# Performance work log

Measured on AMD Instinct MI355X. Metric: run time of the kernel, lower is better.

## Reference

```python
import jax, jax.numpy as jnp
import numpy as np
import math

B, C, N, T = 16, 32, 500, 10
NH, DK = 8, 8
D = NH * DK  # 64
TT = 6       # tem_size after conv_temp1 (10->6)
EPS = 1e-5


def setup_inputs() -> dict:
    key = jax.random.key(0)
    ks = jax.random.split(key, 32)
    s = 0.05
    rn = lambda k, shp: jax.random.normal(k, shp, dtype=jnp.float32) * s
    return {
        "x": jax.random.normal(ks[0], (B, C, N, T), dtype=jnp.float32),
        "A": jax.random.uniform(ks[1], (N, N), dtype=jnp.float32) / N,
        "conv1_W": rn(ks[2], (32, 32)), "conv1_b": jnp.zeros((32,), jnp.float32),
        "te1_W": rn(ks[3], (64, 32)), "te1_b": jnp.zeros((64,), jnp.float32),
        "convq_W": rn(ks[4], (64, 64, 1, 3)), "convq_b": jnp.zeros((64,), jnp.float32),
        "convk_W": rn(ks[5], (64, 64, 1, 3)), "convk_b": jnp.zeros((64,), jnp.float32),
        "linv_W": rn(ks[6], (64, 64)), "linv_b": jnp.zeros((64,), jnp.float32),
        "lino_W": rn(ks[7], (64, 64)), "lino_b": jnp.zeros((64,), jnp.float32),
        "te2_W": rn(ks[8], (32, 64)), "te2_b": jnp.zeros((32,), jnp.float32),
        "mlp_W": rn(ks[9], (64, 160)), "mlp_b": jnp.zeros((64,), jnp.float32),
        "ct1_W": rn(ks[10], (6, 10)), "ct1_b": jnp.zeros((6,), jnp.float32),
        "tat_c1_W": rn(ks[11], (32,)), "tat_c2_W": rn(ks[12], (500,)),
        "tat_w": rn(ks[13], (500, 32)), "tat_b": jnp.zeros((6, 6), jnp.float32),
        "tat_v": rn(ks[14], (6, 6)),
        "bn1_g": jnp.ones((6,), jnp.float32), "bn1_b": jnp.zeros((6,), jnp.float32),
        "bn2_g": jnp.ones((32,), jnp.float32), "bn2_b": jnp.zeros((32,), jnp.float32),
    }


def _forward(x, A, conv1_W, conv1_b, te1_W, te1_b, convq_W, convq_b, convk_W, convk_b,
             linv_W, linv_b, lino_W, lino_b, te2_W, te2_b, mlp_W, mlp_b, ct1_W, ct1_b,
             tat_c1_W, tat_c2_W, tat_w, tat_b, tat_v, bn1_g, bn1_b, bn2_g, bn2_b):
    b, c, n, t = x.shape
    c1x1 = lambda z, W, bb: jnp.einsum('bchw,oc->bohw', z, W) + bb[None, :, None, None]
    residual = c1x1(x, conv1_W, conv1_b)                      # (B,32,N,T)
    h = c1x1(x, te1_W, te1_b)                                 # (B,64,N,T)
    # --- temporal-context multi-head self-attention (att bias is 0 in source due to bug) ---
    dn = ('NCHW', 'OIHW', 'NCHW')
    q = jax.lax.conv_general_dilated(h, convq_W, (1, 1), ((0, 0), (1, 1)), dimension_numbers=dn) + convq_b[None, :, None, None]
    k = jax.lax.conv_general_dilated(h, convk_W, (1, 1), ((0, 0), (1, 1)), dimension_numbers=dn) + convk_b[None, :, None, None]
    sh = lambda z: z.reshape(b, NH, DK, n, t).transpose(0, 3, 1, 4, 2)  # (B,N,h,T,dk)
    q, k = sh(q), sh(k)
    hp = h.transpose(0, 2, 3, 1)                              # (B,N,T,64)
    v = (hp @ linv_W.T + linv_b).reshape(b, n, t, NH, DK).transpose(0, 1, 3, 2, 4)
    p = jax.nn.softmax(jnp.einsum('bnhtd,bnhsd->bnhts', q, k) / math.sqrt(DK), axis=-1)
    o = jnp.einsum('bnhts,bnhsd->bnhtd', p, v).transpose(0, 1, 3, 2, 4).reshape(b, n, t, D)
    h = (o @ lino_W.T + lino_b).transpose(0, 3, 1, 2)         # (B,64,N,T)
    h = c1x1(h, te2_W, te2_b)                                 # (B,32,N,T)
    # --- multi_gcn_d: static adjacency diffusion + per-timestep attention adjacency ---
    co = h.shape[1]
    xt = h.transpose(0, 3, 2, 1)                              # (B,T,N,C)
    att = jax.nn.softmax(jnp.einsum('btnc,btmc->btnm', xt, xt) / math.sqrt(co), axis=-1)
    outs = [h]
    z = jnp.einsum('btvc,wv->btwc', xt, A); outs.append(z.transpose(0, 3, 2, 1))
    z = jnp.einsum('btvc,wv->btwc', z, A);  outs.append(z.transpose(0, 3, 2, 1))
    z = jnp.einsum('btvc,btwv->btwc', xt, att); outs.append(z.transpose(0, 3, 2, 1))
    z = jnp.einsum('btvc,btwv->btwc', z, att);  outs.append(z.transpose(0, 3, 2, 1))
    hc = c1x1(jnp.concatenate(outs, axis=1), mlp_W, mlp_b)    # (B,64,N,T)
    g = jnp.tanh(hc[:, :co]) * jax.nn.sigmoid(hc[:, co:])     # (B,32,N,10)
    # --- conv_temp1: 1x1 conv over the time axis, 10 -> 6 ---
    g = jnp.einsum('bcnt,st->bcns', g, ct1_W) + ct1_b[None, None, None, :]  # (B,32,N,6)
    # --- TATT_1 temporal attention coefficients ---
    f1 = jnp.einsum('bcnt,c->btn', g, tat_c1_W)               # (B,6,N)
    f2 = jnp.einsum('bcnt,n->bct', g, tat_c2_W)               # (B,32,6)
    logits = jax.nn.sigmoid(jnp.einsum('btn,nc,bcs->bts', f1, tat_w, f2) + tat_b)
    logits = jnp.einsum('pt,bts->bps', tat_v, logits)         # (B,6,6)
    lp = logits.transpose(0, 2, 1)
    mu = lp.mean((0, 2), keepdims=True); var = lp.var((0, 2), keepdims=True)
    lp = (lp - mu) / jnp.sqrt(var + EPS) * bn1_g[None, :, None] + bn1_b[None, :, None]
    coefs = jax.nn.softmax(lp.transpose(0, 2, 1), axis=-1)    # (B,6,6)
    Tc = coefs.transpose(0, 2, 1)
    xo = jnp.einsum('bcnl,blq->bcnq', g, Tc)                  # (B,32,N,6)
    xo = jnp.where(xo > 0, xo, 0.01 * xo) + residual[..., -xo.shape[-1]:]
    mu = xo.mean((0, 2, 3), keepdims=True); var = xo.var((0, 2, 3), keepdims=True)
    return (xo - mu) / jnp.sqrt(var + EPS) * bn2_g[None, :, None, None] + bn2_b[None, :, None, None]


def reference(x, A, conv1_W, conv1_b, te1_W, te1_b, convq_W, convq_b, convk_W, convk_b,
              linv_W, linv_b, lino_W, lino_b, te2_W, te2_b, mlp_W, mlp_b, ct1_W, ct1_b,
              tat_c1_W, tat_c2_W, tat_w, tat_b, tat_v, bn1_g, bn1_b, bn2_g, bn2_b):
    return _forward(x, A, conv1_W, conv1_b, te1_W, te1_b, convq_W, convq_b, convk_W, convk_b,
                    linv_W, linv_b, lino_W, lino_b, te2_W, te2_b, mlp_W, mlp_b, ct1_W, ct1_b,
                    tat_c1_W, tat_c2_W, tat_w, tat_b, tat_v, bn1_g, bn1_b, bn2_g, bn2_b)
```

## Files before the change

kernel.cpp:

```cpp
#include <hip/hip_runtime.h>

typedef unsigned short u16;
typedef unsigned int u32;

__device__ __forceinline__ float b2f(u16 v) { return __uint_as_float((u32)v << 16); }
__device__ __forceinline__ float lopart(u32 u) { return __uint_as_float(u << 16); }
__device__ __forceinline__ float hipart(u32 u) { return __uint_as_float(u & 0xffff0000u); }
__device__ __forceinline__ u16 f2b(float f) {
  u32 u = __float_as_uint(f);
  u32 r = u + 0x7fffu + ((u >> 16) & 1u);
  return (u16)(r >> 16);
}
__device__ __forceinline__ u32 pk2(float a, float b) {
  return (u32)f2b(a) | ((u32)f2b(b) << 16);
}
__device__ __forceinline__ u32 cvtpk(float lo, float hi) {
  u32 r;
  asm("v_cvt_pk_bf16_f32 %0, %1, %2" : "=v"(r) : "v"(lo), "v"(hi));
  return r;
}
__device__ __forceinline__ float rd(const void* p, int i, bool BF) {
  return BF ? b2f(((const u16*)p)[i]) : ((const float*)p)[i];
}

struct Ptrs { const void* p[29]; };

typedef __attribute__((ext_vector_type(8))) short short8;
typedef __attribute__((ext_vector_type(4))) float floatx4;

__global__ __launch_bounds__(256) void k_prep(Ptrs ps, float* __restrict__ Wf,
                                              u16* __restrict__ Abf, float* __restrict__ WT,
                                              u16* __restrict__ WBu, float* __restrict__ stats) {
  bool BF = ((*(const u32*)ps.p[25]) & 0xffffu) != 0;
  int blk = blockIdx.x, tid = threadIdx.x;
  const void* p2  = ps.p[2];
  const void* p4  = ps.p[4];
  const void* p5  = ps.p[5];
  const void* p6  = ps.p[6];
  const void* p7  = ps.p[7];
  const void* p8  = ps.p[8];
  const void* p9  = ps.p[9];
  const void* p10 = ps.p[10];
  const void* p11 = ps.p[11];
  const void* p12 = ps.p[12];
  const void* p13 = ps.p[13];
  const void* p14 = ps.p[14];
  const void* p15 = ps.p[15];
  const void* p16 = ps.p[16];
  if (blk < 256) {
    int j = blk * 256 + tid;
    if (j >= 65322) return;
    const int SZ[27] = {1024,32,2048,64,12288,64,12288,64,4096,64,4096,64,2048,32,
                        10240,64,60,6,32,500,16000,36,36,6,6,32,32};
    int t = 0, off = 0;
#pragma unroll
    for (int k = 0; k < 27; ++k) {
      if (t == k && j >= off + SZ[k]) { off += SZ[k]; t = k + 1; }
    }
    Wf[j] = rd(ps.p[2 + t], j - off, BF);
  } else if (blk < 1280) {
    int i = (blk - 256) * 256 + tid;
    int r = i >> 9, v = i & 511;
    bool in = (r < 500) && (v < 500);
    u16 o = 0;
    if (in) o = BF ? ((const u16*)ps.p[1])[r * 500 + v] : f2b(((const float*)ps.p[1])[r * 500 + v]);
    Abf[i] = o;
  } else if (blk < 1366) {
    int i = (blk - 1280) * 256 + tid;
    if (i < 1024) {
      WT[i] = rd(p2, (i & 31) * 32 + (i >> 5), BF);
    } else if (i >= 9600 && i < 9664) {
      int o = i - 9600;
      float s = rd(p11, o, BF);
      for (int i2 = 0; i2 < 64; ++i2)
        s += rd(p10, o * 64 + i2, BF) * rd(p5, i2, BF);
      WT[i] = s;
    } else if (i >= 9664 && i < 11712) {
      int j2 = i - 9664;
      int jj = j2 >> 5, c = j2 & 31;
      float s = 0.f;
      for (int o2 = 0; o2 < 64; ++o2)
        s += rd(p14, c * 64 + o2, BF) * rd(p12, o2 * 64 + jj, BF);
      WT[i] = s;
    } else if (i >= 11712 && i < 11744) {
      int c = i - 11712;
      float s = rd(p15, c, BF);
      for (int o2 = 0; o2 < 64; ++o2)
        s += rd(p14, c * 64 + o2, BF) * rd(p13, o2, BF);
      WT[i] = s;
    } else if (i >= 11744 && i < 21984) {
      int j2 = i - 11744;
      int j = j2 & 7, lanev = (j2 >> 3) & 63, ct = (j2 >> 9) & 3, kt = j2 >> 11;
      int qv = lanev >> 4, lnv = lanev & 15;
      int o = ct * 16 + lnv, k = kt * 32 + qv * 8 + j;
      WBu[j2] = f2b(rd(p16, o * 160 + k, BF));
    }
  } else if (blk < 1390) {
    int idx = (blk - 1366) * 256 + tid;
    int i2 = idx & 3, lanev = (idx >> 2) & 63, mt = (idx >> 8) & 7, ks = idx >> 11;
    int q2 = lanev >> 4, ln = lanev & 15;
    int o = (mt & 3) * 16 + ln;
    const void* src = (mt >= 4) ? p8 : p6;
    int kb0 = q2 * 8 + 2 * i2;
    float v0 = 0.f, v1 = 0.f;
    for (int i3 = 0; i3 < 64; ++i3) {
      float w = rd(src, o * 192 + i3 * 3 + ks, BF);
      v0 += w * rd(p4, i3 * 32 + kb0, BF);
      v1 += w * rd(p4, i3 * 32 + kb0 + 1, BF);
    }
    ((u32*)WT)[22016 + idx] = pk2(v0, v1);
  } else if (blk < 1394) {
    int idx = (blk - 1390) * 256 + tid;
    int i2 = idx & 3, lanev = (idx >> 2) & 63, mt = idx >> 8;
    int o = mt * 16 + (lanev & 15);
    int kb0 = (lanev >> 4) * 8 + 2 * i2;
    float v0 = 0.f, v1 = 0.f;
    for (int i3 = 0; i3 < 64; ++i3) {
      float w = rd(p10, o * 64 + i3, BF);
      v0 += w * rd(p4, i3 * 32 + kb0, BF);
      v1 += w * rd(p4, i3 * 32 + kb0 + 1, BF);
    }
    ((u32*)WT)[28160 + idx] = pk2(v0, v1);
  } else if (blk < 1397) {
    int j = (blk - 1394) * 256 + tid;
    if (j < 768) {
      bool isK = j >= 384;
      int jj = isK ? j - 384 : j;
      int cls = jj >> 6, o = jj & 63;
      const void* srcW = isK ? p8 : p6;
      const void* srcB = isK ? p9 : p7;
      float S0 = 0.f, S1 = 0.f, S2 = 0.f;
      for (int i3 = 0; i3 < 64; ++i3) {
        float tb = rd(p5, i3, BF);
        S0 += rd(srcW, o * 192 + i3 * 3 + 0, BF) * tb;
        S1 += rd(srcW, o * 192 + i3 * 3 + 1, BF) * tb;
        S2 += rd(srcW, o * 192 + i3 * 3 + 2, BF) * tb;
      }
      float val = rd(srcB, o, BF) + S1 + (cls > 0 ? S0 : 0.f) + (cls < 2 ? S2 : 0.f);
      WT[29184 + j] = val;
    }
  } else {
    if (tid < 64) stats[tid] = 0.f;
  }
}

__global__ __launch_bounds__(256, 4) void k_a2m(const u16* __restrict__ Abf,
                                                u16* __restrict__ A2bf) {
  __shared__ u32 blsT[8192];
  int tid = threadIdx.x;
  int c0 = blockIdx.x * 32;
  for (int i = tid; i < 8192; i += 256) {
    int c = i & 31, h = i >> 5;
    int r0 = 2 * h;
    u32 lo = Abf[r0 * 512 + c0 + c];
    u32 hi = Abf[(r0 + 1) * 512 + c0 + c];
    blsT[c * 256 + (((h & 0xFC) ^ ((c & 15) << 2)) | (h & 3))] = lo | (hi << 16);
  }
  __syncthreads();
  int lane = tid & 63, wave = tid >> 6;
  int q = lane >> 4, ln = lane & 15;
  int rbase = blockIdx.y * 64 + wave * 16;
  const u32* Au = (const u32*)Abf;
  int arow = (rbase + ln) * 256;
  union F8 { u32 u[4]; short8 s; };
  floatx4 acc[2] = {{0.f,0.f,0.f,0.f},{0.f,0.f,0.f,0.f}};
  for (int c2 = 0; c2 < 16; ++c2) {
    int hb = c2 * 16 + q * 4;
    F8 af;
#pragma unroll
    for (int i2 = 0; i2 < 4; ++i2) af.u[i2] = Au[arow + hb + i2];
#pragma unroll
    for (int t2 = 0; t2 < 2; ++t2) {
      int c = t2 * 16 + ln;
      int baseT = c * 256 + (hb ^ ((c & 15) << 2));
      F8 bf;
#pragma unroll
      for (int i2 = 0; i2 < 4; ++i2) bf.u[i2] = blsT[baseT + i2];
      acc[t2] = __builtin_amdgcn_mfma_f32_16x16x32_bf16(af.s, bf.s, acc[t2], 0, 0, 0);
    }
  }
#pragma unroll
  for (int t2 = 0; t2 < 2; ++t2) {
#pragma unroll
    for (int i2 = 0; i2 < 4; ++i2) {
      int r = rbase + q * 4 + i2;
      A2bf[r * 512 + c0 + t2 * 16 + ln] = f2b(acc[t2][i2]);
    }
  }
}

__global__ __launch_bounds__(256, 5) void k_front3(
    const void* __restrict__ xraw, const void* __restrict__ g1, const float* __restrict__ WT,
    const float* __restrict__ c1B,
    float* __restrict__ h3x, float* __restrict__ res6)
{
  __shared__ __align__(16) float arena[4][1680];
  int tid = threadIdx.x;
  int wave = tid >> 6, lane = tid & 63;
  float* Aw = arena[wave];
  int pair = blockIdx.x * 4 + wave;
  int b = pair / 500, n = pair - b * 500;

  const float* c1T  = WT;
  const float* bvp  = WT + 9600;
  const float* otT  = WT + 9664;
  const float* botp = WT + 11712;
  const u32* WQKf = (const u32*)WT + 22016;
  const u32* WVf  = (const u32*)WT + 28160;
  const float* bq3 = WT + 29184;
  const float* bk3 = WT + 29568;

  {
    bool BF = ((*(const u32*)g1) & 0xffffu) != 0;
    int c0 = lane >> 1, hf = (lane & 1) * 5;
    int base = ((b * 32 + c0) * 500 + n) * 10 + hf;
    float* dst = Aw + c0 * 12 + hf;
    if (BF) {
      const u16* xp = (const u16*)xraw + base;
#pragma unroll
      for (int k2 = 0; k2 < 5; ++k2) dst[k2] = b2f(xp[k2]);
    } else {
      const float* xp = (const float*)xraw + base;
#pragma unroll
      for (int k2 = 0; k2 < 5; ++k2) dst[k2] = xp[k2];
    }
  }
  __builtin_amdgcn_wave_barrier();

  int cl = lane & 31, th = lane >> 5;
  int q2 = lane >> 4, ln15 = lane & 15;

  {
    float r0 = c1B[cl], r1 = r0, r2 = r0;
#pragma unroll 4
    for (int i = 0; i < 32; ++i) {
      float w = c1T[i * 32 + cl];
      const float* xr = Aw + i * 12 + 4 + th * 3;
      r0 += w * xr[0]; r1 += w * xr[1]; r2 += w * xr[2];
    }
    float* rp = res6 + ((b * 32 + cl) * 500 + n) * 6 + th * 3;
    rp[0] = r0; rp[1] = r1; rp[2] = r2;
  }

  {
    u32* xT3u = (u32*)Aw + 384;
    for (int e = lane; e < 480; e += 64) {
      int t = e / 48, col2 = e - t * 48;
      int kk0 = col2 * 2, kk1 = kk0 + 1;
      int tau0 = kk0 >> 5, c0 = kk0 & 31;
      int tau1 = kk1 >> 5, c1 = kk1 & 31;
      int tx0 = t - 1 + tau0, tx1 = t - 1 + tau1;
      float f0 = (tx0 >= 0 && tx0 < 10) ? Aw[c0 * 12 + tx0] : 0.f;
      float f1 = (tx1 >= 0 && tx1 < 10) ? Aw[c1 * 12 + tx1] : 0.f;
      xT3u[t * 52 + col2] = cvtpk(f0, f1);
    }
  }
  __builtin_amdgcn_wave_barrier();

  union F8 { u32 u[4]; short8 s; };
  floatx4 aq[4] = {{0.f,0.f,0.f,0.f},{0.f,0.f,0.f,0.f},{0.f,0.f,0.f,0.f},{0.f,0.f,0.f,0.f}};
  floatx4 ak[4] = {{0.f,0.f,0.f,0.f},{0.f,0.f,0.f,0.f},{0.f,0.f,0.f,0.f},{0.f,0.f,0.f,0.f}};
  floatx4 av[4] = {{0.f,0.f,0.f,0.f},{0.f,0.f,0.f,0.f},{0.f,0.f,0.f,0.f},{0.f,0.f,0.f,0.f}};
  {
    const u32* xT3u = (const u32*)Aw + 384;
#pragma unroll
    for (int ks = 0; ks < 3; ++ks) {
      F8 bfr;
      const u32* bp = xT3u + ln15 * 52 + ks * 16 + q2 * 4;
#pragma unroll
      for (int i2 = 0; i2 < 4; ++i2) bfr.u[i2] = bp[i2];
#pragma unroll
      for (int mt = 0; mt < 4; ++mt) {
        F8 afr;
        const u32* ap = WQKf + ((ks * 8 + mt) * 64 + lane) * 4;
#pragma unroll
        for (int i2 = 0; i2 < 4; ++i2) afr.u[i2] = ap[i2];
        aq[mt] = __builtin_amdgcn_mfma_f32_16x16x32_bf16(afr.s, bfr.s, aq[mt], 0, 0, 0);
      }
#pragma unroll
      for (int mt = 0; mt < 4; ++mt) {
        F8 afr;
        const u32* ap = WQKf + ((ks * 8 + 4 + mt) * 64 + lane) * 4;
#pragma unroll
        for (int i2 = 0; i2 < 4; ++i2) afr.u[i2] = ap[i2];
        ak[mt] = __builtin_amdgcn_mfma_f32_16x16x32_bf16(afr.s, bfr.s, ak[mt], 0, 0, 0);
      }
      if (ks == 1) {
#pragma unroll
        for (int mt = 0; mt < 4; ++mt) {
          F8 afr;
          const u32* ap = WVf + (mt * 64 + lane) * 4;
#pragma unroll
          for (int i2 = 0; i2 < 4; ++i2) afr.u[i2] = ap[i2];
          av[mt] = __builtin_amdgcn_mfma_f32_16x16x32_bf16(afr.s, bfr.s, av[mt], 0, 0, 0);
        }
      }
    }
  }
  __builtin_amdgcn_wave_barrier();
  if (ln15 < 10) {
    int t = ln15;
    int cls = (t == 0) ? 0 : ((t == 9) ? 2 : 1);
    const float* bq = bq3 + cls * 64;
    const float* bk = bk3 + cls * 64;
    u16* q16 = (u16*)Aw;
    u16* k16 = (u16*)((u32*)Aw + 320);
    u16* v16 = (u16*)((u32*)Aw + 960);
#pragma unroll
    for (int mt = 0; mt < 4; ++mt) {
#pragma unroll
      for (int i2 = 0; i2 < 4; ++i2) {
        int o = mt * 16 + q2 * 4 + i2;
        q16[o * 10 + t] = f2b(aq[mt][i2] + bq[o]);
        k16[o * 10 + t] = f2b(ak[mt][i2] + bk[o]);
        v16[o * 10 + t] = f2b(av[mt][i2] + bvp[o]);
      }
    }
  }
  __builtin_amdgcn_wave_barrier();

  {
    const u32* qb = (const u32*)Aw;
    const u32* kb = (const u32*)Aw + 320;
#pragma unroll
    for (int pass = 0; pass < 2; ++pass) {
      int row = pass * 64 + lane;
      if (row < 80) {
        int h8 = (row / 10) * 8, r = row - (row / 10) * 10;
        int rm = r >> 1, rs = r & 1;
        float sv[10];
#pragma unroll
        for (int s = 0; s < 10; ++s) sv[s] = 0.f;
#pragma unroll 2
        for (int d = 0; d < 8; ++d) {
          int jj = h8 + d;
          u32 qu = qb[jj * 5 + rm];
          float qv = rs ? hipart(qu) : lopart(qu);
          const u32* kp2 = kb + jj * 5;
          u32 ka0 = kp2[0], ka1 = kp2[1], ka2 = kp2[2], ka3 = kp2[3], ka4 = kp2[4];
          sv[0] += qv * lopart(ka0); sv[1] += qv * hipart(ka0);
          sv[2] += qv * lopart(ka1); sv[3] += qv * hipart(ka1);
          sv[4] += qv * lopart(ka2); sv[5] += qv * hipart(ka2);
          sv[6] += qv * lopart(ka3); sv[7] += qv * hipart(ka3);
          sv[8] += qv * lopart(ka4); sv[9] += qv * hipart(ka4);
        }
        const float sc_ = 0.35355339059327373f;
        float mx = sv[0];
#pragma unroll
        for (int s = 1; s < 10; ++s) mx = fmaxf(mx, sv[s]);
        float tot = 0.f, ev[10];
#pragma unroll
        for (int s = 0; s < 10; ++s) { ev[s] = __expf((sv[s] - mx) * sc_); tot += ev[s]; }
        float inv = 1.f / tot;
        u32* pp = (u32*)Aw + 1280 + row * 5;
#pragma unroll
        for (int m2 = 0; m2 < 5; ++m2)
          pp[m2] = cvtpk(ev[2 * m2] * inv, ev[2 * m2 + 1] * inv);
      }
    }
  }
  __builtin_amdgcn_wave_barrier();

  {
    float vrL[10];
    const u32* vp = (const u32*)Aw + 960 + lane * 5;
#pragma unroll
    for (int m2 = 0; m2 < 5; ++m2) {
      u32 w = vp[m2];
      vrL[2 * m2] = lopart(w); vrL[2 * m2 + 1] = hipart(w);
    }
    const u32* pb = (const u32*)Aw + 1280 + (lane >> 3) * 50;
    float orr[10];
#pragma unroll
    for (int t = 0; t < 10; ++t) {
      const u32* pr = pb + t * 5;
      float a = 0.f;
#pragma unroll
      for (int m2 = 0; m2 < 5; ++m2) {
        u32 w = pr[m2];
        a += lopart(w) * vrL[2 * m2] + hipart(w) * vrL[2 * m2 + 1];
      }
      orr[t] = a;
    }
    float* op = Aw + lane * 12;
    *(float4*)op       = make_float4(orr[0], orr[1], orr[2], orr[3]);
    *(float4*)(op + 4) = make_float4(orr[4], orr[5], orr[6], orr[7]);
    *(float2*)(op + 8) = make_float2(orr[8], orr[9]);
  }
  __builtin_amdgcn_wave_barrier();

  {
    float bt2 = botp[cl];
    float a5[5];
#pragma unroll
    for (int k2 = 0; k2 < 5; ++k2) a5[k2] = bt2;
    const float* tp0 = otT + cl;
    const float* base = Aw + th * 5;
#pragma unroll 2
    for (int j = 0; j < 64; ++j) {
      float w = tp0[j * 32];
      const float* lp = base + j * 12;
#pragma unroll
      for (int k2 = 0; k2 < 5; ++k2) a5[k2] += w * lp[k2];
    }
    int t0 = th * 5;
#pragma unroll
    for (int k2 = 0; k2 < 5; ++k2)
      h3x[((b * 10 + t0 + k2) * 500 + n) * 32 + cl] = a5[k2];
  }
}

__global__ __launch_bounds__(256, 4) void k_z12m(const float* __restrict__ h3x,
    const u16* __restrict__ Abf, const u16* __restrict__ A2bf,
    float* __restrict__ z1x, float* __restrict__ z2x) {
  __shared__ u32 xlsT[8192];
  int tid = threadIdx.x, bt = blockIdx.x;
  const float* src = h3x + bt * 16000;
  for (int i = tid; i < 8192; i += 256) {
    int n = i & 31, h = i >> 5;
    int r0 = 2 * h;
    float v0 = (r0 < 500) ? src[r0 * 32 + n] : 0.f;
    float v1 = (r0 + 1 < 500) ? src[(r0 + 1) * 32 + n] : 0.f;
    xlsT[n * 256 + (((h & 0xFC) ^ ((n & 15) << 2)) | (h & 3))] = cvtpk(v0, v1);
  }
  __syncthreads();
  int lane = tid & 63, wave = tid >> 6;
  int q = lane >> 4, ln = lane & 15;
  int rbase = blockIdx.y * 64 + wave * 16;
  const u32* Au = (const u32*)Abf;
  const u32* A2u = (const u32*)A2bf;
  int arow = (rbase + ln) * 256;
  union F8 { u32 u[4]; short8 s; };
  floatx4 acc1[2] = {{0.f,0.f,0.f,0.f},{0.f,0.f,0.f,0.f}};
  floatx4 acc2[2] = {{0.f,0.f,0.f,0.f},{0.f,0.f,0.f,0.f}};
  for (int c2 = 0; c2 < 16; ++c2) {
    int hb = c2 * 16 + q * 4;
    F8 a1f, a2f;
#pragma unroll
    for (int i2 = 0; i2 < 4; ++i2) {
      a1f.u[i2] = Au[arow + hb + i2];
      a2f.u[i2] = A2u[arow + hb + i2];
    }
#pragma unroll
    for (int t2 = 0; t2 < 2; ++t2) {
      int n = t2 * 16 + ln;
      int baseT = n * 256 + (hb ^ ((n & 15) << 2));
      F8 bf;
#pragma unroll
      for (int i2 = 0; i2 < 4; ++i2) bf.u[i2] = xlsT[baseT + i2];
      acc1[t2] = __builtin_amdgcn_mfma_f32_16x16x32_bf16(a1f.s, bf.s, acc1[t2], 0, 0, 0);
      acc2[t2] = __builtin_amdgcn_mfma_f32_16x16x32_bf16(a2f.s, bf.s, acc2[t2], 0, 0, 0);
    }
  }
  int outb = bt * 16000;
#pragma unroll
  for (int t2 = 0; t2 < 2; ++t2) {
#pragma unroll
    for (int i2 = 0; i2 < 4; ++i2) {
      int r = rbase + q * 4 + i2;
      if (r < 500) {
        z1x[outb + r * 32 + t2 * 16 + ln] = acc1[t2][i2];
        z2x[outb + r * 32 + t2 * 16 + ln] = acc2[t2][i2];
      }
    }
  }
}

__global__ __launch_bounds__(256, 2) void k_attn2(const float* __restrict__ keys,
                                                  const float* __restrict__ vals,
                                                  float* __restrict__ outp) {
  __shared__ u32 kls[10240];
  __shared__ u32 vls[8192];
  __shared__ u32 aux[1216];
  int tid = threadIdx.x, bt = blockIdx.x, yh = blockIdx.y;
  const float* kb = keys + bt * 16000;
  const float* vb = vals + bt * 16000;
  for (int i = tid; i < 8192; i += 256) {
    int r = i >> 4, cu = i & 15;
    float2 g = make_float2(0.f, 0.f);
    if (r < 500) g = *(const float2*)(kb + r * 32 + cu * 2);
    kls[r * 20 + cu] = cvtpk(g.x, g.y);
    int n = i & 31, h = i >> 5;
    int r0 = 2 * h;
    float v0 = (r0 < 500) ? vb[r0 * 32 + n] : 0.f;
    float v1 = (r0 + 1 < 500) ? vb[(r0 + 1) * 32 + n] : 0.f;
    vls[n * 256 + (((h & 0xFC) ^ ((n & 15) << 2)) | (h & 3))] = cvtpk(v0, v1);
  }
  __syncthreads();
  int lane = tid & 63, wave = tid >> 6;
  int q = lane >> 4, ln = lane & 15;
  int wrow = wave >> 1, ch = wave & 1;
  float* smx = (float*)(aux + 1088);
  float* sms = (float*)(aux + 1152);
  u32* myp = aux + wave * 272;
  float* zex = (float*)aux;
  u16* pw = (u16*)myp;
  union F8 { u32 u[4]; short8 s; };
  const float sc = 0.17677669529663687f;
  int outb = bt * 16000;
  for (int chunk = 0; chunk < 8; ++chunk) {
    int rbase = yh * 256 + chunk * 32 + wrow * 16;
    F8 af;
    {
      int r = rbase + ln;
      int wbase = r * 20 + q * 4;
#pragma unroll
      for (int i2 = 0; i2 < 4; ++i2)
        af.u[i2] = kls[wbase + i2];
    }
    floatx4 acc[16];
#pragma unroll
    for (int ctl = 0; ctl < 16; ++ctl) {
      int r2 = (ch * 16 + ctl) * 16 + ln;
      int wb2 = r2 * 20 + q * 4;
      F8 bf;
#pragma unroll
      for (int i2 = 0; i2 < 4; ++i2)
        bf.u[i2] = kls[wb2 + i2];
      acc[ctl] = __builtin_amdgcn_mfma_f32_16x16x32_bf16(af.s, bf.s,
                (floatx4){0.f, 0.f, 0.f, 0.f}, 0, 0, 0);
    }
    if (ch == 1 && ln >= 4) {
#pragma unroll
      for (int i2 = 0; i2 < 4; ++i2) acc[15][i2] = -1e30f;
    }
    float m[4];
#pragma unroll
    for (int i2 = 0; i2 < 4; ++i2) {
      float mm = -1e30f;
#pragma unroll
      for (int ctl = 0; ctl < 16; ++ctl) mm = fmaxf(mm, acc[ctl][i2]);
#pragma unroll
      for (int d = 1; d < 16; d <<= 1) mm = fmaxf(mm, __shfl_xor(mm, d));
      m[i2] = mm;
    }
    if (ln == 0) {
#pragma unroll
      for (int i2 = 0; i2 < 4; ++i2) smx[wave * 16 + q * 4 + i2] = m[i2];
    }
    __syncthreads();
    float sp[4];
#pragma unroll
    for (int i2 = 0; i2 < 4; ++i2) {
      float mm = fmaxf(m[i2], smx[(wave ^ 1) * 16 + q * 4 + i2]);
      float s = 0.f;
#pragma unroll
      for (int ctl = 0; ctl < 16; ++ctl) {
        float e = __expf((acc[ctl][i2] - mm) * sc);
        acc[ctl][i2] = e; s += e;
      }
#pragma unroll
      for (int d = 1; d < 16; d <<= 1) s += __shfl_xor(s, d);
      sp[i2] = s;
    }
    if (ln == 0) {
#pragma unroll
      for (int i2 = 0; i2 < 4; ++i2) sms[wave * 16 + q * 4 + i2] = sp[i2];
    }
    __syncthreads();
    float inv[4];
#pragma unroll
    for (int i2 = 0; i2 < 4; ++i2)
      inv[i2] = 1.f / (sp[i2] + sms[(wave ^ 1) * 16 + q * 4 + i2]);
    floatx4 zacc[2] = {{0.f,0.f,0.f,0.f},{0.f,0.f,0.f,0.f}};
    for (int c2l = 0; c2l < 8; ++c2l) {
#pragma unroll
      for (int t2 = 0; t2 < 2; ++t2) {
        int ctl = c2l * 2 + t2;
#pragma unroll
        for (int i2 = 0; i2 < 4; ++i2)
          pw[(q * 4 + i2) * 34 + t2 * 16 + ln] = f2b(acc[ctl][i2]);
      }
      __builtin_amdgcn_wave_barrier();
      F8 pa;
#pragma unroll
      for (int i2 = 0; i2 < 4; ++i2) pa.u[i2] = myp[ln * 17 + q * 4 + i2];
      int hb = (ch * 8 + c2l) * 16 + q * 4;
#pragma unroll
      for (int t2 = 0; t2 < 2; ++t2) {
        int n = t2 * 16 + ln;
        int baseT = n * 256 + (hb ^ ((n & 15) << 2));
        F8 bf;
#pragma unroll
        for (int i2 = 0; i2 < 4; ++i2) bf.u[i2] = vls[baseT + i2];
        zacc[t2] = __builtin_amdgcn_mfma_f32_16x16x32_bf16(pa.s, bf.s, zacc[t2], 0, 0, 0);
      }
      __builtin_amdgcn_wave_barrier();
    }
    __syncthreads();
    if (ch) {
#pragma unroll
      for (int t2 = 0; t2 < 2; ++t2)
#pragma unroll
        for (int i2 = 0; i2 < 4; ++i2)
          zex[wrow * 544 + (q * 4 + i2) * 34 + t2 * 16 + ln] = zacc[t2][i2];
    }
    __syncthreads();
    if (!ch) {
#pragma unroll
      for (int t2 = 0; t2 < 2; ++t2) {
#pragma unroll
        for (int i2 = 0; i2 < 4; ++i2) {
          int r = rbase + q * 4 + i2;
          if (r < 500) {
            float vsum = zacc[t2][i2] + zex[wrow * 544 + (q * 4 + i2) * 34 + t2 * 16 + ln];
            outp[outb + r * 32 + t2 * 16 + ln] = vsum * inv[i2];
          }
        }
      }
    }
  }
}

__global__ __launch_bounds__(256, 2) void k_gate(
    const float* __restrict__ h3x, const float* __restrict__ z1x, const float* __restrict__ z2x,
    const float* __restrict__ z3x, const float* __restrict__ z4x,
    const u32* __restrict__ WBq, const float* __restrict__ mlpB,
    const float* __restrict__ ct1W, const float* __restrict__ ct1B,
    float* __restrict__ g2w)
{
  __shared__ u32 wlds[5120];
  int tid = threadIdx.x;
  for (int i = tid; i < 5120; i += 256) wlds[i] = WBq[i];
  __syncthreads();
  int lane = tid & 63, wave = tid >> 6;
  int q = lane >> 4, ln = lane & 15;
  int b = blockIdx.y;
  int n0 = blockIdx.x * 32 + wave * 8;
  int nA = n0 + (ln & 7);
  int tAb = ln >> 3;
  int nD = n0 + (q & 1) * 4;
  int tDb = q >> 1;
  float g2a[4][2][6];
#pragma unroll
  for (int i = 0; i < 4; ++i)
#pragma unroll
    for (int ch = 0; ch < 2; ++ch)
#pragma unroll
      for (int s = 0; s < 6; ++s) g2a[i][ch][s] = 0.f;
  float bias[4];
#pragma unroll
  for (int ct = 0; ct < 4; ++ct) bias[ct] = mlpB[ct * 16 + ln];
  union F8 { u32 u[4]; short8 s; };
  for (int tile = 0; tile < 5; ++tile) {
    int tA = tile * 2 + tAb;
    int offA = (((b * 10 + tA) * 500) + nA) * 32 + q * 8;
    floatx4 acc[4];
#pragma unroll
    for (int ct = 0; ct < 4; ++ct) acc[ct] = (floatx4){bias[ct], bias[ct], bias[ct], bias[ct]};
#pragma unroll
    for (int kt = 0; kt < 5; ++kt) {
      const float* sp = kt == 0 ? h3x : kt == 1 ? z1x : kt == 2 ? z2x : kt == 3 ? z3x : z4x;
      float4 a0 = *(const float4*)(sp + offA);
      float4 a1 = *(const float4*)(sp + offA + 4);
      F8 af;
      af.u[0] = cvtpk(a0.x, a0.y);
      af.u[1] = cvtpk(a0.z, a0.w);
      af.u[2] = cvtpk(a1.x, a1.y);
      af.u[3] = cvtpk(a1.z, a1.w);
#pragma unroll
      for (int ct = 0; ct < 4; ++ct) {
        F8 bfr;
        const u32* wp = wlds + (((kt * 4 + ct) << 6) + lane) * 4;
#pragma unroll
        for (int i2 = 0; i2 < 4; ++i2) bfr.u[i2] = wp[i2];
        acc[ct] = __builtin_amdgcn_mfma_f32_16x16x32_bf16(af.s, bfr.s, acc[ct], 0, 0, 0);
      }
    }
    int tD = tile * 2 + tDb;
    float c6[6];
#pragma unroll
    for (int s = 0; s < 6; ++s) c6[s] = ct1W[s * 10 + tD];
#pragma unroll
    for (int i = 0; i < 4; ++i) {
      float e0 = __expf(2.f * acc[0][i]);
      float g0 = ((e0 - 1.f) / (e0 + 1.f)) * (1.f / (1.f + __expf(-acc[2][i])));
      float e1 = __expf(2.f * acc[1][i]);
      float g1 = ((e1 - 1.f) / (e1 + 1.f)) * (1.f / (1.f + __expf(-acc[3][i])));
#pragma unroll
      for (int s = 0; s < 6; ++s) {
        g2a[i][0][s] += g0 * c6[s];
        g2a[i][1][s] += g1 * c6[s];
      }
    }
  }
#pragma unroll
  for (int i = 0; i < 4; ++i)
#pragma unroll
    for (int ch = 0; ch < 2; ++ch)
#pragma unroll
      for (int s = 0; s < 6; ++s)
        g2a[i][ch][s] += __shfl_xor(g2a[i][ch][s], 32);
  if (q < 2) {
#pragma unroll
    for (int i = 0; i < 4; ++i) {
      int n = nD + i;
      if (n < 500) {
#pragma unroll
        for (int ch = 0; ch < 2; ++ch) {
          int c = ln + ch * 16;
          float* gp = g2w + ((b * 32 + c) * 500 + n) * 6;
#pragma unroll
          for (int s = 0; s < 6; ++s) gp[s] = g2a[i][ch][s] + ct1B[s];
        }
      }
    }
  }
}

__global__ __launch_bounds__(256) void k_f12(const float* __restrict__ g2w,
                                             const float* __restrict__ tc1W,
                                             const float* __restrict__ c2W,
                                             float* __restrict__ f1w, float* __restrict__ f2w) {
  int blk = blockIdx.x, tid = threadIdx.x;
  if (blk < 188) {
    int i = blk * 256 + tid;
    if (i >= 48000) return;
    int b = i / 3000, rem = i - b * 3000, s = rem / 500, n = rem - s * 500;
    float a = 0.f;
    for (int c = 0; c < 32; ++c) a += g2w[((b * 32 + c) * 500 + n) * 6 + s] * tc1W[c];
    f1w[(b * 6 + s) * 500 + n] = a;
  } else {
    int pb = (blk - 188) * 4 + (tid >> 6);
    int b = pb >> 5, c = pb & 31, lane = tid & 63;
    float acc[6];
#pragma unroll
    for (int t = 0; t < 6; ++t) acc[t] = 0.f;
    for (int n = lane; n < 500; n += 64) {
      float w = c2W[n];
      const float* gp = g2w + ((b * 32 + c) * 500 + n) * 6;
#pragma unroll
      for (int t = 0; t < 6; ++t) acc[t] += w * gp[t];
    }
#pragma unroll
    for (int t = 0; t < 6; ++t)
      for (int off = 32; off; off >>= 1) acc[t] += __shfl_xor(acc[t], off);
    if (lane == 0) {
#pragma unroll
      for (int t = 0; t < 6; ++t) f2w[(b * 32 + c) * 6 + t] = acc[t];
    }
  }
}

__global__ __launch_bounds__(256) void k_tatt(
    const float* __restrict__ f1w, const float* __restrict__ tatw,
    const float* __restrict__ f2w, const float* __restrict__ tatb, const float* __restrict__ tatv,
    float* __restrict__ lg2w)
{
  __shared__ float mid[192];
  __shared__ float lgt[36];
  int b = blockIdx.x, tid = threadIdx.x;
  if (tid < 192) {
    int t = tid >> 5, c = tid & 31;
    float a = 0.f;
    const float* f1p = f1w + (b * 6 + t) * 500;
    for (int n = 0; n < 500; ++n) a += f1p[n] * tatw[n * 32 + c];
    mid[t * 32 + c] = a;
  }
  __syncthreads();
  if (tid < 36) {
    int t = tid / 6, s = tid - t * 6;
    float a = tatb[t * 6 + s];
    for (int c = 0; c < 32; ++c) a += mid[t * 32 + c] * f2w[(b * 32 + c) * 6 + s];
    lgt[t * 6 + s] = 1.f / (1.f + expf(-a));
  }
  __syncthreads();
  if (tid < 36) {
    int p = tid / 6, s = tid - p * 6;
    float a = 0.f;
#pragma unroll
    for (int t2 = 0; t2 < 6; ++t2) a += tatv[p * 6 + t2] * lgt[t2 * 6 + s];
    lg2w[(b * 6 + p) * 6 + s] = a;
  }
}

__global__ __launch_bounds__(128) void k_coefs(const float* __restrict__ lg2w,
    const float* __restrict__ bn1g, const float* __restrict__ bn1b, float* __restrict__ tcw) {
  __shared__ float mu[6], iv[6], gg[6], bb[6];
  int tid = threadIdx.x;
  if (tid < 6) {
    float s = 0.f, sq = 0.f;
    for (int b = 0; b < 16; ++b)
      for (int q = 0; q < 6; ++q) {
        float v = lg2w[(b * 6 + q) * 6 + tid];
        s += v; sq += v * v;
      }
    float m = s / 96.f;
    mu[tid] = m;
    iv[tid] = rsqrtf(sq / 96.f - m * m + 1e-5f);
    gg[tid] = bn1g[tid]; bb[tid] = bn1b[tid];
  }
  __syncthreads();
  for (int idx = tid; idx < 96; idx += 128) {
    int b = idx / 6, q = idx - b * 6;
    float v[6], mx = -1e30f;
#pragma unroll
    for (int l = 0; l < 6; ++l) {
      v[l] = (lg2w[(b * 6 + q) * 6 + l] - mu[l]) * iv[l] * gg[l] + bb[l];
      mx = fmaxf(mx, v[l]);
    }
    float tot = 0.f;
#pragma unroll
    for (int l = 0; l < 6; ++l) { v[l] = expf(v[l] - mx); tot += v[l]; }
    float inv = 1.f / tot;
#pragma unroll
    for (int l = 0; l < 6; ++l) tcw[(b * 6 + l) * 6 + q] = v[l] * inv;
  }
}

__global__ __launch_bounds__(256) void k_xo(const float* __restrict__ g2w,
    const float* __restrict__ res6, const float* __restrict__ tcw,
    float* __restrict__ xow, float* __restrict__ stats) {
  __shared__ float Tcl[36];
  __shared__ float redS[32][8], redQ[32][8];
  int b = blockIdx.x, chunk = blockIdx.y, tid = threadIdx.x;
  if (tid < 36) Tcl[tid] = tcw[b * 36 + tid];
  __syncthreads();
  int c = tid & 31, sub = tid >> 5;
  int n0 = chunk * 50;
  float s = 0.f, sq = 0.f;
  for (int idx = sub; idx < 300; idx += 8) {
    int nl = idx / 6, q = idx - nl * 6;
    int n = n0 + nl;
    int base = ((b * 32 + c) * 500 + n) * 6;
    const float* gp = g2w + base;
    float xv = 0.f;
#pragma unroll
    for (int l = 0; l < 6; ++l) xv += gp[l] * Tcl[l * 6 + q];
    xv = xv > 0.f ? xv : 0.01f * xv;
    xv += res6[base + q];
    xow[base + q] = xv;
    s += xv; sq += xv * xv;
  }
  redS[c][sub] = s; redQ[c][sub] = sq;
  __syncthreads();
  if (sub == 0) {
    float ts = 0.f, tq = 0.f;
#pragma unroll
    for (int k = 0; k < 8; ++k) { ts += redS[c][k]; tq += redQ[c][k]; }
    atomicAdd(&stats[c], ts);
    atomicAdd(&stats[32 + c], tq);
  }
}

__global__ __launch_bounds__(256) void k_out(const float* __restrict__ xow,
    const float* __restrict__ stats, const float* __restrict__ g2c, const float* __restrict__ b2c,
    float* __restrict__ out) {
  int base = (blockIdx.x * 256 + threadIdx.x) * 4;
#pragma unroll
  for (int k = 0; k < 4; ++k) {
    int i = base + k;
    int c = (i / 3000) & 31;
    float m = stats[c] * (1.f / 48000.f);
    float var = stats[32 + c] * (1.f / 48000.f) - m * m;
    out[i] = (xow[i] - m) * rsqrtf(var + 1e-5f) * g2c[c] + b2c[c];
  }
}

extern "C" void kernel_launch(void* const* d_in, const int* in_sizes, int n_in,
                              void* d_out, int out_size, void* d_ws, size_t ws_size,
                              hipStream_t stream)
{
  (void)in_sizes; (void)out_size;

  float* ws = (float*)d_ws;
  float* Af   = ws;
  float* Wf   = Af + 250000;
  float* A2   = Wf + 65536;
  float* h3x  = A2 + 250000;
  float* z1x  = h3x + 2560000;
  float* z2x  = z1x + 2560000;
  float* z3x  = z2x + 2560000;
  float* z4x  = z3x + 2560000;
  float* res6 = z4x + 2560000;
  float* g2w  = res6 + 1536000;
  float* f1w  = g2w + 1536000;
  float* f2w  = f1w + 48000;
  float* lg2w = f2w + 3072;
  float* tcw  = lg2w + 576;
  float* stats= tcw + 576;
  float* xow  = z1x;
  u16*   Abf  = (u16*)g2w;
  u16*   A2bf = (u16*)(g2w + 131072);
  float* WTp  = g2w + 262144;
  u16*   WBu  = (u16*)f1w;
  if (ws_size < (size_t)16489952 * sizeof(float)) return;

  const float* c1B  = Wf + 1024;
  const float* mlpB = Wf + 48512;
  const float* ct1W = Wf + 48576;
  const float* ct1B = Wf + 48636;
  const float* tc1W = Wf + 48642;
  const float* tc2W = Wf + 48674;
  const float* tatw = Wf + 49174;
  const float* tatb = Wf + 65174;
  const float* tatv = Wf + 65210;
  const float* bn1g = Wf + 65246;
  const float* bn1b = Wf + 65252;
  const float* bn2g = Wf + 65258;
  const float* bn2b = Wf + 65290;

  Ptrs ps;
  for (int i = 0; i < 29; ++i) ps.p[i] = (i < n_in) ? d_in[i] : d_in[0];

  k_prep <<<dim3(1398),    256, 0, stream>>>(ps, Wf, Abf, WTp, WBu, stats);
  k_a2m  <<<dim3(16, 8),   256, 0, stream>>>(Abf, A2bf);
  k_front3<<<dim3(2000),   256, 0, stream>>>(ps.p[0], ps.p[25], WTp, c1B, h3x, res6);
  k_z12m <<<dim3(160, 8),  256, 0, stream>>>(h3x, Abf, A2bf, z1x, z2x);
  k_attn2<<<dim3(160, 2),  256, 0, stream>>>(h3x, h3x, z3x);
  k_attn2<<<dim3(160, 2),  256, 0, stream>>>(h3x, z3x, z4x);
  k_gate <<<dim3(16, 16),  256, 0, stream>>>(h3x, z1x, z2x, z3x, z4x,
                                             (const u32*)WBu, mlpB, ct1W, ct1B, g2w);
  k_f12  <<<dim3(316),     256, 0, stream>>>(g2w, tc1W, tc2W, f1w, f2w);
  k_tatt <<<dim3(16),      256, 0, stream>>>(f1w, tatw, f2w, tatb, tatv, lg2w);
  k_coefs<<<dim3(1),       128, 0, stream>>>(lg2w, bn1g, bn1b, tcw);
  k_xo   <<<dim3(16, 10),  256, 0, stream>>>(g2w, res6, tcw, xow, stats);
  k_out  <<<dim3(1500),    256, 0, stream>>>(xow, stats, bn2g, bn2b, (float*)d_out);
}
```

Measured before the change: 391.9 us.

## Use per-wave online softmax in attention to remove cross-wave reductions

Before, k_attn2 split each 16-row query tile's key range across two waves, which had to exchange max, sum and partial outputs through shared memory with several block-wide barriers per chunk. Now each wave owns its query rows and walks both key halves itself, using an online-softmax rescale (running max and sum) so no inter-wave exchange or __syncthreads is needed in the loop. This removes barrier stalls and shared-memory traffic, at the cost of a longer serial chain per wave and an extra exp/rescale per row.

```diff
diff --git a/kernel.cpp b/kernel.cpp
--- a/kernel.cpp
+++ b/kernel.cpp
@@ -471,7 +471,7 @@
                                                   float* __restrict__ outp) {
   __shared__ u32 kls[10240];
   __shared__ u32 vls[8192];
-  __shared__ u32 aux[1216];
+  __shared__ u32 pch[1088];
   int tid = threadIdx.x, bt = blockIdx.x, yh = blockIdx.y;
   const float* kb = keys + bt * 16000;
   const float* vb = vals + bt * 16000;
@@ -489,124 +489,98 @@
   __syncthreads();
   int lane = tid & 63, wave = tid >> 6;
   int q = lane >> 4, ln = lane & 15;
-  int wrow = wave >> 1, ch = wave & 1;
-  float* smx = (float*)(aux + 1088);
-  float* sms = (float*)(aux + 1152);
-  u32* myp = aux + wave * 272;
-  float* zex = (float*)aux;
+  u32* myp = pch + wave * 272;
   u16* pw = (u16*)myp;
   union F8 { u32 u[4]; short8 s; };
   const float sc = 0.17677669529663687f;
   int outb = bt * 16000;
-  for (int chunk = 0; chunk < 8; ++chunk) {
-    int rbase = yh * 256 + chunk * 32 + wrow * 16;
+  for (int chunk = 0; chunk < 4; ++chunk) {
+    int rbase = yh * 256 + chunk * 64 + wave * 16;
     F8 af;
     {
       int r = rbase + ln;
       int wbase = r * 20 + q * 4;
 #pragma unroll
-      for (int i2 = 0; i2 < 4; ++i2)
-        af.u[i2] = kls[wbase + i2];
-    }
-    floatx4 acc[16];
-#pragma unroll
-    for (int ctl = 0; ctl < 16; ++ctl) {
-      int r2 = (ch * 16 + ctl) * 16 + ln;
-      int wb2 = r2 * 20 + q * 4;
-      F8 bf;
-#pragma unroll
-      for (int i2 = 0; i2 < 4; ++i2)
-        bf.u[i2] = kls[wb2 + i2];
-      acc[ctl] = __builtin_amdgcn_mfma_f32_16x16x32_bf16(af.s, bf.s,
-                (floatx4){0.f, 0.f, 0.f, 0.f}, 0, 0, 0);
-    }
-    if (ch == 1 && ln >= 4) {
-#pragma unroll
-      for (int i2 = 0; i2 < 4; ++i2) acc[15][i2] = -1e30f;
-    }
-    float m[4];
-#pragma unroll
-    for (int i2 = 0; i2 < 4; ++i2) {
-      float mm = -1e30f;
-#pragma unroll
-      for (int ctl = 0; ctl < 16; ++ctl) mm = fmaxf(mm, acc[ctl][i2]);
-#pragma unroll
-      for (int d = 1; d < 16; d <<= 1) mm = fmaxf(mm, __shfl_xor(mm, d));
-      m[i2] = mm;
-    }
-    if (ln == 0) {
-#pragma unroll
-      for (int i2 = 0; i2 < 4; ++i2) smx[wave * 16 + q * 4 + i2] = m[i2];
-    }
-    __syncthreads();
-    float sp[4];
-#pragma unroll
-    for (int i2 = 0; i2 < 4; ++i2) {
-      float mm = fmaxf(m[i2], smx[(wave ^ 1) * 16 + q * 4 + i2]);
-      float s = 0.f;
+      for (int i2 = 0; i2 < 4; ++i2) af.u[i2] = kls[wbase + i2];
+    }
+    floatx4 zacc[2] = {{0.f,0.f,0.f,0.f},{0.f,0.f,0.f,0.f}};
+    float mrun[4], srun[4];
+#pragma unroll 1
+    for (int kh = 0; kh < 2; ++kh) {
+      floatx4 acc[16];
 #pragma unroll
       for (int ctl = 0; ctl < 16; ++ctl) {
-        float e = __expf((acc[ctl][i2] - mm) * sc);
-        acc[ctl][i2] = e; s += e;
-      }
-#pragma unroll
-      for (int d = 1; d < 16; d <<= 1) s += __shfl_xor(s, d);
-      sp[i2] = s;
-    }
-    if (ln == 0) {
-#pragma unroll
-      for (int i2 = 0; i2 < 4; ++i2) sms[wave * 16 + q * 4 + i2] = sp[i2];
-    }
-    __syncthreads();
+        int r2 = (kh * 16 + ctl) * 16 + ln;
+        int wb2 = r2 * 20 + q * 4;
+        F8 bf;
+#pragma unroll
+        for (int i2 = 0; i2 < 4; ++i2) bf.u[i2] = kls[wb2 + i2];
+        acc[ctl] = __builtin_amdgcn_mfma_f32_16x16x32_bf16(af.s, bf.s,
+                  (floatx4){0.f, 0.f, 0.f, 0.f}, 0, 0, 0);
+      }
+      if (kh == 1 && ln >= 4) {
+#pragma unroll
+        for (int i2 = 0; i2 < 4; ++i2) acc[15][i2] = -1e30f;
+      }
+#pragma unroll
+      for (int i2 = 0; i2 < 4; ++i2) {
+        float mm = -1e30f;
+#pragma unroll
+        for (int ctl = 0; ctl < 16; ++ctl) mm = fmaxf(mm, acc[ctl][i2]);
+#pragma unroll
+        for (int d = 1; d < 16; d <<= 1) mm = fmaxf(mm, __shfl_xor(mm, d));
+        float M, r0s;
+        if (kh == 0) { M = mm; r0s = 1.f; }
+        else { M = fmaxf(mrun[i2], mm); r0s = __expf((mrun[i2] - M) * sc); }
+        float s = 0.f;
+#pragma unroll
+        for (int ctl = 0; ctl < 16; ++ctl) {
+          float e = __expf((acc[ctl][i2] - M) * sc);
+          acc[ctl][i2] = e; s += e;
+        }
+#pragma unroll
+        for (int d = 1; d < 16; d <<= 1) s += __shfl_xor(s, d);
+        if (kh == 0) { mrun[i2] = M; srun[i2] = s; }
+        else {
+          srun[i2] = srun[i2] * r0s + s;
+          zacc[0][i2] *= r0s;
+          zacc[1][i2] *= r0s;
+        }
+      }
+      for (int c2l = 0; c2l < 8; ++c2l) {
+#pragma unroll
+        for (int t2 = 0; t2 < 2; ++t2) {
+          int ctl = c2l * 2 + t2;
+#pragma unroll
+          for (int i2 = 0; i2 < 4; ++i2)
+            pw[(q * 4 + i2) * 34 + t2 * 16 + ln] = f2b(acc[ctl][i2]);
+        }
+        __builtin_amdgcn_wave_barrier();
+        F8 pa;
+#pragma unroll
+        for (int i2 = 0; i2 < 4; ++i2) pa.u[i2] = myp[ln * 17 + q * 4 + i2];
+        int hb = (kh * 8 + c2l) * 16 + q * 4;
+#pragma unroll
+        for (int t2 = 0; t2 < 2; ++t2) {
+          int n = t2 * 16 + ln;
+          int baseT = n * 256 + (hb ^ ((n & 15) << 2));
+          F8 bf;
+#pragma unroll
+          for (int i2 = 0; i2 < 4; ++i2) bf.u[i2] = vls[baseT + i2];
+          zacc[t2] = __builtin_amdgcn_mfma_f32_16x16x32_bf16(pa.s, bf.s, zacc[t2], 0, 0, 0);
+        }
+        __builtin_amdgcn_wave_barrier();
+      }
+    }
     float inv[4];
 #pragma unroll
-    for (int i2 = 0; i2 < 4; ++i2)
-      inv[i2] = 1.f / (sp[i2] + sms[(wave ^ 1) * 16 + q * 4 + i2]);
-    floatx4 zacc[2] = {{0.f,0.f,0.f,0.f},{0.f,0.f,0.f,0.f}};
-    for (int c2l = 0; c2l < 8; ++c2l) {
-#pragma unroll
-      for (int t2 = 0; t2 < 2; ++t2) {
-        int ctl = c2l * 2 + t2;
-#pragma unroll
-        for (int i2 = 0; i2 < 4; ++i2)
-          pw[(q * 4 + i2) * 34 + t2 * 16 + ln] = f2b(acc[ctl][i2]);
-      }
-      __builtin_amdgcn_wave_barrier();
-      F8 pa;
-#pragma unroll
-      for (int i2 = 0; i2 < 4; ++i2) pa.u[i2] = myp[ln * 17 + q * 4 + i2];
-      int hb = (ch * 8 + c2l) * 16 + q * 4;
-#pragma unroll
-      for (int t2 = 0; t2 < 2; ++t2) {
-        int n = t2 * 16 + ln;
-        int baseT = n * 256 + (hb ^ ((n & 15) << 2));
-        F8 bf;
-#pragma unroll
-        for (int i2 = 0; i2 < 4; ++i2) bf.u[i2] = vls[baseT + i2];
-        zacc[t2] = __builtin_amdgcn_mfma_f32_16x16x32_bf16(pa.s, bf.s, zacc[t2], 0, 0, 0);
-      }
-      __builtin_amdgcn_wave_barrier();
-    }
-    __syncthreads();
-    if (ch) {
-#pragma unroll
-      for (int t2 = 0; t2 < 2; ++t2)
-#pragma unroll
-        for (int i2 = 0; i2 < 4; ++i2)
-          zex[wrow * 544 + (q * 4 + i2) * 34 + t2 * 16 + ln] = zacc[t2][i2];
-    }
-    __syncthreads();
-    if (!ch) {
-#pragma unroll
-      for (int t2 = 0; t2 < 2; ++t2) {
-#pragma unroll
-        for (int i2 = 0; i2 < 4; ++i2) {
-          int r = rbase + q * 4 + i2;
-          if (r < 500) {
-            float vsum = zacc[t2][i2] + zex[wrow * 544 + (q * 4 + i2) * 34 + t2 * 16 + ln];
-            outp[outb + r * 32 + t2 * 16 + ln] = vsum * inv[i2];
-          }
-        }
+    for (int i2 = 0; i2 < 4; ++i2) inv[i2] = 1.f / srun[i2];
+#pragma unroll
+    for (int t2 = 0; t2 < 2; ++t2) {
+#pragma unroll
+      for (int i2 = 0; i2 < 4; ++i2) {
+        int r = rbase + q * 4 + i2;
+        if (r < 500) outp[outb + r * 32 + t2 * 16 + ln] = zacc[t2][i2] * inv[i2];
       }
     }
   }
```

Result: no change. 386.3 us (-1.4%).
